# Kernel tuning notes

Measured on AMD Instinct MI355X. Metric: run time of the kernel, lower is better.

Reference implementation:

```python
import jax, jax.numpy as jnp
import numpy as np

D_MODEL = 1024
NUM_HEADS = 16
MAX_LEN = 2048
HEAD_DIM = D_MODEL // NUM_HEADS
BATCH = 4
SEQ = 1024


def setup_inputs() -> dict:
    key = jax.random.key(0)
    ks = jax.random.split(key, 5)
    return {
        "query": jax.random.normal(ks[0], (BATCH, SEQ, D_MODEL), dtype=jnp.float32),
        "key": jax.random.normal(ks[1], (BATCH, SEQ, D_MODEL), dtype=jnp.float32),
        "value": jax.random.normal(ks[2], (BATCH, SEQ, D_MODEL), dtype=jnp.float32),
        "rel_k": jax.random.normal(ks[3], (MAX_LEN, HEAD_DIM), dtype=jnp.float32),
        "rel_v": jax.random.normal(ks[4], (MAX_LEN, HEAD_DIM), dtype=jnp.float32),
    }


def reference(query, key, value, rel_k, rel_v):
    B, S, D = query.shape
    H, hd = NUM_HEADS, D // NUM_HEADS
    # (B, H, S, hd)
    q = query.reshape(B, S, H, hd).transpose(0, 2, 1, 3)
    k = key.reshape(B, S, H, hd).transpose(0, 2, 1, 3)
    v = value.reshape(B, S, H, hd).transpose(0, 2, 1, 3)
    scale = 1.0 / np.sqrt(hd).astype(np.float32)
    # content scores + relative-position key bias (q . rel_k)
    scores = jnp.einsum("bhqd,bhkd->bhqk", q, k) * scale
    scores = scores + jnp.einsum("bhqd,kd->bhqk", q, rel_k[:S])
    attn = jax.nn.softmax(scores, axis=-1)  # (B, H, S, S)
    out = jnp.einsum("bhqk,bhkd->bhqd", attn, v)
    out = out + jnp.einsum("bhqk,kd->bhqd", attn, rel_v[:S])
    return out.transpose(0, 2, 1, 3).reshape(B, S, D)
```

## Files before the change

### kernel.cpp

```cpp
#include <hip/hip_runtime.h>

#define SQ 1024
#define DM 1024
#define HD 64
#define NBH 64

typedef __attribute__((ext_vector_type(8))) _Float16 v8h;
typedef __attribute__((ext_vector_type(4))) float v4f;
typedef __attribute__((ext_vector_type(2))) __fp16 v2fp16;
typedef __attribute__((ext_vector_type(4))) unsigned int v4u;

typedef __attribute__((address_space(3))) void as3_void;
typedef __attribute__((address_space(1))) const void as1_cvoid;

__device__ __forceinline__ v4f mfma_f16(v8h a, v8h b, v4f c) {
  return __builtin_amdgcn_mfma_f32_16x16x32_f16(a, b, c, 0, 0, 0);
}

__device__ __forceinline__ void gload16(const _Float16* g, v8h* l) {
  __builtin_amdgcn_global_load_lds((as1_cvoid*)g, (as3_void*)l, 16, 0, 0);
}

__global__ __launch_bounds__(256) void prep_kernel(
    const float* __restrict__ q, const float* __restrict__ k, const float* __restrict__ v,
    const float* __restrict__ relk, const float* __restrict__ relv,
    _Float16* __restrict__ Qh, _Float16* __restrict__ Kh,
    _Float16* __restrict__ Vth)
{
  __shared__ float vt[64][65];
  int blk = blockIdx.x;
  int st = blk & 15;
  int bh = blk >> 4;
  int b = bh >> 4, h = bh & 15;
  int s0 = st * 64;
  int t = (int)threadIdx.x;
  int d = t & 63, sl4 = t >> 6;
  const float scale = 0.125f;

  #pragma unroll
  for (int i = 0; i < 16; ++i) {
    int sl = sl4 + i * 4;
    int s = s0 + sl;
    size_t gidx = ((size_t)(b * SQ + s)) * DM + h * HD + d;
    float qv = q[gidx];
    float kv = k[gidx] * scale + relk[s * HD + d];
    float vv = v[gidx] + relv[s * HD + d];
    size_t widx = ((size_t)(bh * SQ + s)) * HD + d;
    Qh[widx] = (_Float16)qv;
    Kh[widx] = (_Float16)kv;
    vt[sl][d] = vv;
  }
  __syncthreads();
  int sl = t & 63, d4 = t >> 6;
  #pragma unroll
  for (int i = 0; i < 16; ++i) {
    int dd = d4 + i * 4;
    Vth[((size_t)(bh * HD + dd)) * SQ + s0 + sl] = (_Float16)vt[sl][dd];
  }
}

__global__ __launch_bounds__(256) void attn_kernel(
    const _Float16* __restrict__ Qh, const _Float16* __restrict__ Kh,
    const _Float16* __restrict__ Vth, float* __restrict__ out)
{
  __shared__ v8h KlG[2][512];
  __shared__ v8h VlG[2][512];

  int tid = (int)threadIdx.x;
  int lane = tid & 63, w = tid >> 6;
  int g = lane >> 4, r15 = lane & 15;
  int bid = (int)blockIdx.x;
  int wk = (bid & 7) * 64 + (bid >> 3);
  int bh = wk >> 3, qt = wk & 7;
  int b = bh >> 4, h = bh & 15;
  int q0 = qt * 128 + w * 32;

  v8h aq[2][2];
  #pragma unroll
  for (int t = 0; t < 2; ++t) {
    const _Float16* qb = Qh + ((size_t)(bh * SQ + q0 + 16 * t + r15)) * HD;
    aq[t][0] = *(const v8h*)(qb + g * 8);
    aq[t][1] = *(const v8h*)(qb + 32 + g * 8);
  }

  const _Float16* kb = Kh + (size_t)bh * SQ * HD;
  const _Float16* vb = Vth + (size_t)bh * HD * SQ;

  size_t kOff[2], vOff[2];
  int ldsG[2];
  #pragma unroll
  for (int j = 0; j < 2; ++j) {
    int G = w * 128 + j * 64 + lane;
    int row = G >> 3, gr = G & 7;
    int fs = (row & 3) | (((row >> 3) & 1) << 2);
    int src = gr ^ fs;
    kOff[j] = (size_t)row * HD + src * 8;
    vOff[j] = (size_t)row * SQ + src * 8;
    ldsG[j] = w * 128 + j * 64;
  }

  v4f o[2][4];
  #pragma unroll
  for (int t = 0; t < 2; ++t)
    #pragma unroll
    for (int c = 0; c < 4; ++c) o[t][c] = (v4f){0.f, 0.f, 0.f, 0.f};
  float m[2] = {-3.0e38f, -3.0e38f}, l[2] = {0.f, 0.f};

  int krow[4];
  #pragma unroll
  for (int c = 0; c < 4; ++c)
    krow[c] = ((c >> 1) << 5) + ((r15 >> 2) << 3) + ((c & 1) << 2) + (r15 & 3);
  int fk = (r15 & 3) | (((r15 >> 2) & 1) << 2);
  int fv = (r15 & 3) | (((r15 >> 3) & 1) << 2);

  #pragma unroll
  for (int j = 0; j < 2; ++j) {
    gload16(kb + kOff[j], &KlG[0][ldsG[j]]);
    gload16(vb + vOff[j], &VlG[0][ldsG[j]]);
  }
  __syncthreads();

  for (int t0 = 0; t0 < SQ / 64; ++t0) {
    int cur = t0 & 1;
    if (t0 < SQ / 64 - 1) {
      size_t kT = (size_t)(t0 + 1) * 64 * HD;
      size_t vT = (size_t)(t0 + 1) * 64;
      #pragma unroll
      for (int j = 0; j < 2; ++j) {
        gload16(kb + kT + kOff[j], &KlG[cur ^ 1][ldsG[j]]);
        gload16(vb + vT + vOff[j], &VlG[cur ^ 1][ldsG[j]]);
      }
    }

    v4f s[2][4];
    #pragma unroll
    for (int c = 0; c < 4; ++c) {
      v8h kf0 = KlG[cur][krow[c] * 8 + (g ^ fk)];
      v8h kf1 = KlG[cur][krow[c] * 8 + ((4 | g) ^ fk)];
      v4f z0 = (v4f){0.f, 0.f, 0.f, 0.f};
      v4f z1 = (v4f){0.f, 0.f, 0.f, 0.f};
      z0 = mfma_f16(kf0, aq[0][0], z0);
      z0 = mfma_f16(kf1, aq[0][1], z0);
      z1 = mfma_f16(kf0, aq[1][0], z1);
      z1 = mfma_f16(kf1, aq[1][1], z1);
      s[0][c] = z0;
      s[1][c] = z1;
    }

    #pragma unroll
    for (int t = 0; t < 2; ++t) {
      float pm = s[t][0][0];
      #pragma unroll
      for (int c = 0; c < 4; ++c)
        #pragma unroll
        for (int r = 0; r < 4; ++r)
          pm = fmaxf(pm, s[t][c][r]);
      if (!__all(pm - m[t] <= 8.f)) {
        pm = fmaxf(pm, __shfl_xor(pm, 16));
        pm = fmaxf(pm, __shfl_xor(pm, 32));
        float mnew = fmaxf(m[t], pm);
        float sc = __expf(m[t] - mnew);
        m[t] = mnew;
        l[t] *= sc;
        #pragma unroll
        for (int c = 0; c < 4; ++c) o[t][c] *= sc;
      }
      float rs = 0.f;
      #pragma unroll
      for (int c = 0; c < 4; ++c)
        #pragma unroll
        for (int r = 0; r < 4; ++r) {
          float p = __expf(s[t][c][r] - m[t]);
          s[t][c][r] = p;
          rs += p;
        }
      l[t] += rs;
    }

    v8h pb0[2], pb1[2];
    #pragma unroll
    for (int t = 0; t < 2; ++t) {
      v4u w0, w1;
      w0[0] = __builtin_bit_cast(unsigned int, __builtin_amdgcn_cvt_pkrtz(s[t][0][0], s[t][0][1]));
      w0[1] = __builtin_bit_cast(unsigned int, __builtin_amdgcn_cvt_pkrtz(s[t][0][2], s[t][0][3]));
      w0[2] = __builtin_bit_cast(unsigned int, __builtin_amdgcn_cvt_pkrtz(s[t][1][0], s[t][1][1]));
      w0[3] = __builtin_bit_cast(unsigned int, __builtin_amdgcn_cvt_pkrtz(s[t][1][2], s[t][1][3]));
      w1[0] = __builtin_bit_cast(unsigned int, __builtin_amdgcn_cvt_pkrtz(s[t][2][0], s[t][2][1]));
      w1[1] = __builtin_bit_cast(unsigned int, __builtin_amdgcn_cvt_pkrtz(s[t][2][2], s[t][2][3]));
      w1[2] = __builtin_bit_cast(unsigned int, __builtin_amdgcn_cvt_pkrtz(s[t][3][0], s[t][3][1]));
      w1[3] = __builtin_bit_cast(unsigned int, __builtin_amdgcn_cvt_pkrtz(s[t][3][2], s[t][3][3]));
      pb0[t] = __builtin_bit_cast(v8h, w0);
      pb1[t] = __builtin_bit_cast(v8h, w1);
    }

    #pragma unroll
    for (int c = 0; c < 4; ++c) {
      int rv = 16 * c + r15;
      v8h vf0 = VlG[cur][rv * 8 + (g ^ fv)];
      v8h vf1 = VlG[cur][rv * 8 + ((4 | g) ^ fv)];
      #pragma unroll
      for (int t = 0; t < 2; ++t) {
        o[t][c] = mfma_f16(vf0, pb0[t], o[t][c]);
        o[t][c] = mfma_f16(vf1, pb1[t], o[t][c]);
      }
    }

    __syncthreads();
  }

  #pragma unroll
  for (int t = 0; t < 2; ++t) {
    float lr = l[t];
    lr += __shfl_xor(lr, 16);
    lr += __shfl_xor(lr, 32);
    float inv = 1.f / lr;
    int qrow = q0 + 16 * t + r15;
    #pragma unroll
    for (int c = 0; c < 4; ++c) {
      v4f res = o[t][c] * inv;
      *(v4f*)(&out[((size_t)(b * SQ + qrow)) * DM + h * HD + 16 * c + 4 * g]) = res;
    }
  }
}

extern "C" void kernel_launch(void* const* d_in, const int* in_sizes, int n_in,
                              void* d_out, int out_size, void* d_ws, size_t ws_size,
                              hipStream_t stream) {
  const float* q = (const float*)d_in[0];
  const float* k = (const float*)d_in[1];
  const float* v = (const float*)d_in[2];
  const float* relk = (const float*)d_in[3];
  const float* relv = (const float*)d_in[4];

  _Float16* Qh = (_Float16*)d_ws;
  _Float16* Kh = Qh + (size_t)NBH * SQ * HD;
  _Float16* Vth = Kh + (size_t)NBH * SQ * HD;

  prep_kernel<<<dim3(NBH * (SQ / 64)), dim3(256), 0, stream>>>(q, k, v, relk, relv, Qh, Kh, Vth);
  attn_kernel<<<dim3(512), dim3(256), 0, stream>>>(Qh, Kh, Vth, (float*)d_out);
}
```

Measured before the change: 50.42 us.

## Triple-buffer K/V tiles and software-pipeline QK^T one tile ahead of softmax

Moves from double to triple LDS buffering so global loads are issued two tiles ahead, and computes the QK^T scores for the next tile before the softmax and PV of the current tile. The aim is to hide global-load latency and overlap MFMA score work with the exp/softmax VALU work. It costs extra LDS (one more K and V buffer), more live registers for the second score set, and modulo-3 buffer indexing, which could lower occupancy.

```diff
diff --git a/kernel.cpp b/kernel.cpp
--- a/kernel.cpp
+++ b/kernel.cpp
@@ -59,12 +59,29 @@
   }
 }
 
+#define QK_TILE(S, BUFBASE)                                        \
+  {                                                                \
+    _Pragma("unroll")                                              \
+    for (int c = 0; c < 4; ++c) {                                  \
+      v8h kf0 = KlG[(BUFBASE) + krow[c] * 8 + (g ^ fk)];           \
+      v8h kf1 = KlG[(BUFBASE) + krow[c] * 8 + ((4 | g) ^ fk)];     \
+      v4f z0 = (v4f){0.f, 0.f, 0.f, 0.f};                          \
+      v4f z1 = (v4f){0.f, 0.f, 0.f, 0.f};                          \
+      z0 = mfma_f16(kf0, aq[0][0], z0);                            \
+      z0 = mfma_f16(kf1, aq[0][1], z0);                            \
+      z1 = mfma_f16(kf0, aq[1][0], z1);                            \
+      z1 = mfma_f16(kf1, aq[1][1], z1);                            \
+      S[0][c] = z0;                                                \
+      S[1][c] = z1;                                                \
+    }                                                              \
+  }
+
 __global__ __launch_bounds__(256) void attn_kernel(
     const _Float16* __restrict__ Qh, const _Float16* __restrict__ Kh,
     const _Float16* __restrict__ Vth, float* __restrict__ out)
 {
-  __shared__ v8h KlG[2][512];
-  __shared__ v8h VlG[2][512];
+  __shared__ v8h KlG[3 * 512];
+  __shared__ v8h VlG[3 * 512];
 
   int tid = (int)threadIdx.x;
   int lane = tid & 63, w = tid >> 6;
@@ -113,48 +130,47 @@
   int fk = (r15 & 3) | (((r15 >> 2) & 1) << 2);
   int fv = (r15 & 3) | (((r15 >> 3) & 1) << 2);
 
+  const int NT = SQ / 64;
+
   #pragma unroll
   for (int j = 0; j < 2; ++j) {
-    gload16(kb + kOff[j], &KlG[0][ldsG[j]]);
-    gload16(vb + vOff[j], &VlG[0][ldsG[j]]);
+    gload16(kb + kOff[j], &KlG[ldsG[j]]);
+    gload16(vb + vOff[j], &VlG[ldsG[j]]);
+  }
+  #pragma unroll
+  for (int j = 0; j < 2; ++j) {
+    gload16(kb + (size_t)64 * HD + kOff[j], &KlG[512 + ldsG[j]]);
+    gload16(vb + 64 + vOff[j], &VlG[512 + ldsG[j]]);
   }
   __syncthreads();
 
-  for (int t0 = 0; t0 < SQ / 64; ++t0) {
-    int cur = t0 & 1;
-    if (t0 < SQ / 64 - 1) {
-      size_t kT = (size_t)(t0 + 1) * 64 * HD;
-      size_t vT = (size_t)(t0 + 1) * 64;
+  v4f s_cur[2][4], s_next[2][4];
+  QK_TILE(s_cur, 0);
+
+  #pragma unroll 2
+  for (int t0 = 0; t0 < NT; ++t0) {
+    int bstage = (t0 + 2) % 3, bnext = (t0 + 1) % 3, bcur = t0 % 3;
+
+    if (t0 + 2 < NT) {
+      size_t kT = (size_t)(t0 + 2) * 64 * HD;
+      size_t vT = (size_t)(t0 + 2) * 64;
       #pragma unroll
       for (int j = 0; j < 2; ++j) {
-        gload16(kb + kT + kOff[j], &KlG[cur ^ 1][ldsG[j]]);
-        gload16(vb + vT + vOff[j], &VlG[cur ^ 1][ldsG[j]]);
+        gload16(kb + kT + kOff[j], &KlG[bstage * 512 + ldsG[j]]);
+        gload16(vb + vT + vOff[j], &VlG[bstage * 512 + ldsG[j]]);
       }
     }
 
-    v4f s[2][4];
-    #pragma unroll
-    for (int c = 0; c < 4; ++c) {
-      v8h kf0 = KlG[cur][krow[c] * 8 + (g ^ fk)];
-      v8h kf1 = KlG[cur][krow[c] * 8 + ((4 | g) ^ fk)];
-      v4f z0 = (v4f){0.f, 0.f, 0.f, 0.f};
-      v4f z1 = (v4f){0.f, 0.f, 0.f, 0.f};
-      z0 = mfma_f16(kf0, aq[0][0], z0);
-      z0 = mfma_f16(kf1, aq[0][1], z0);
-      z1 = mfma_f16(kf0, aq[1][0], z1);
-      z1 = mfma_f16(kf1, aq[1][1], z1);
-      s[0][c] = z0;
-      s[1][c] = z1;
-    }
+    if (t0 + 1 < NT) QK_TILE(s_next, bnext * 512);
 
     #pragma unroll
     for (int t = 0; t < 2; ++t) {
-      float pm = s[t][0][0];
+      float pm = s_cur[t][0][0];
       #pragma unroll
       for (int c = 0; c < 4; ++c)
         #pragma unroll
         for (int r = 0; r < 4; ++r)
-          pm = fmaxf(pm, s[t][c][r]);
+          pm = fmaxf(pm, s_cur[t][c][r]);
       if (!__all(pm - m[t] <= 8.f)) {
         pm = fmaxf(pm, __shfl_xor(pm, 16));
         pm = fmaxf(pm, __shfl_xor(pm, 32));
@@ -170,8 +186,8 @@
       for (int c = 0; c < 4; ++c)
         #pragma unroll
         for (int r = 0; r < 4; ++r) {
-          float p = __expf(s[t][c][r] - m[t]);
-          s[t][c][r] = p;
+          float p = __expf(s_cur[t][c][r] - m[t]);
+          s_cur[t][c][r] = p;
           rs += p;
         }
       l[t] += rs;
@@ -181,14 +197,14 @@
     #pragma unroll
     for (int t = 0; t < 2; ++t) {
       v4u w0, w1;
-      w0[0] = __builtin_bit_cast(unsigned int, __builtin_amdgcn_cvt_pkrtz(s[t][0][0], s[t][0][1]));
-      w0[1] = __builtin_bit_cast(unsigned int, __builtin_amdgcn_cvt_pkrtz(s[t][0][2], s[t][0][3]));
-      w0[2] = __builtin_bit_cast(unsigned int, __builtin_amdgcn_cvt_pkrtz(s[t][1][0], s[t][1][1]));
-      w0[3] = __builtin_bit_cast(unsigned int, __builtin_amdgcn_cvt_pkrtz(s[t][1][2], s[t][1][3]));
-      w1[0] = __builtin_bit_cast(unsigned int, __builtin_amdgcn_cvt_pkrtz(s[t][2][0], s[t][2][1]));
-      w1[1] = __builtin_bit_cast(unsigned int, __builtin_amdgcn_cvt_pkrtz(s[t][2][2], s[t][2][3]));
-      w1[2] = __builtin_bit_cast(unsigned int, __builtin_amdgcn_cvt_pkrtz(s[t][3][0], s[t][3][1]));
-      w1[3] = __builtin_bit_cast(unsigned int, __builtin_amdgcn_cvt_pkrtz(s[t][3][2], s[t][3][3]));
+      w0[0] = __builtin_bit_cast(unsigned int, __builtin_amdgcn_cvt_pkrtz(s_cur[t][0][0], s_cur[t][0][1]));
+      w0[1] = __builtin_bit_cast(unsigned int, __builtin_amdgcn_cvt_pkrtz(s_cur[t][0][2], s_cur[t][0][3]));
+      w0[2] = __builtin_bit_cast(unsigned int, __builtin_amdgcn_cvt_pkrtz(s_cur[t][1][0], s_cur[t][1][1]));
+      w0[3] = __builtin_bit_cast(unsigned int, __builtin_amdgcn_cvt_pkrtz(s_cur[t][1][2], s_cur[t][1][3]));
+      w1[0] = __builtin_bit_cast(unsigned int, __builtin_amdgcn_cvt_pkrtz(s_cur[t][2][0], s_cur[t][2][1]));
+      w1[1] = __builtin_bit_cast(unsigned int, __builtin_amdgcn_cvt_pkrtz(s_cur[t][2][2], s_cur[t][2][3]));
+      w1[2] = __builtin_bit_cast(unsigned int, __builtin_amdgcn_cvt_pkrtz(s_cur[t][3][0], s_cur[t][3][1]));
+      w1[3] = __builtin_bit_cast(unsigned int, __builtin_amdgcn_cvt_pkrtz(s_cur[t][3][2], s_cur[t][3][3]));
       pb0[t] = __builtin_bit_cast(v8h, w0);
       pb1[t] = __builtin_bit_cast(v8h, w1);
     }
@@ -196,8 +212,8 @@
     #pragma unroll
     for (int c = 0; c < 4; ++c) {
       int rv = 16 * c + r15;
-      v8h vf0 = VlG[cur][rv * 8 + (g ^ fv)];
-      v8h vf1 = VlG[cur][rv * 8 + ((4 | g) ^ fv)];
+      v8h vf0 = VlG[bcur * 512 + rv * 8 + (g ^ fv)];
+      v8h vf1 = VlG[bcur * 512 + rv * 8 + ((4 | g) ^ fv)];
       #pragma unroll
       for (int t = 0; t < 2; ++t) {
         o[t][c] = mfma_f16(vf0, pb0[t], o[t][c]);
@@ -206,6 +222,12 @@
     }
 
     __syncthreads();
+
+    #pragma unroll
+    for (int t = 0; t < 2; ++t)
+      #pragma unroll
+      for (int c = 0; c < 4; ++c)
+        s_cur[t][c] = s_next[t][c];
   }
 
   #pragma unroll
```

Result: no change. 50.14 us (-0.5%).
